# Optimization experiments

Measured on AMD Instinct MI355X. Metric: run time of the kernel, lower is better.

The kernel has to match this reference:

```python
import jax, jax.numpy as jnp
import numpy as np

MAX_SAMPLES = 400  # init max_samples
EPS = 1e-9


def setup_inputs() -> dict:
    key = jax.random.key(0)
    k1, k2, k3, k4 = jax.random.split(key, 4)
    E, N, K, L = 8192, 2048, 8, 16
    # per-edge probabilities (positive, as the loss takes log of ratios)
    probas = jax.random.uniform(k1, (E,), jnp.float32, minval=1e-3, maxval=1.0)
    # soft cluster assignments: row-normalized so Bhattacharyya coeff <= 1
    c = jax.random.uniform(k2, (N, K), jnp.float32)
    clusters = c / c.sum(axis=1, keepdims=True)
    edges_nn = jax.random.randint(k3, (E, 2), 0, N)
    label_keypoints = jax.random.randint(k4, (L,), 0, N)
    return {"probas": probas, "clusters": clusters,
            "edges_nn": edges_nn, "label_keypoints": label_keypoints}


def reference(probas, clusters, edges_nn, label_keypoints):
    E = edges_nn.shape[0]
    clst = jnp.argmax(clusters, axis=1)                      # [N] hard assignment
    c0 = clst[edges_nn[:, 0]]                                # [E]
    c1 = clst[edges_nn[:, 1]]                                # [E]
    assigned = clst[label_keypoints]                         # [L] clusters at keypoints
    # edge selected if either endpoint lies in a keypoint cluster (union over labels,
    # static-shape mask form of get_edges_on_location)
    sel = jnp.any((c0[None, :] == assigned[:, None]) |
                  (c1[None, :] == assigned[:, None]), axis=0)  # [E]
    sims = c0 == c1
    pos = sel & sims                                          # positive edges
    neg = sel & ~sims                                         # negative edges
    # Bhattacharyya coefficient per edge: sum_k sqrt(p_k * q_k)
    bc = jnp.sqrt(clusters[edges_nn[:, 0]] * clusters[edges_nn[:, 1]]).sum(axis=1)  # [E]
    # pos x neg cross product, restricted to pairs sharing the anchor node edges[.,0]
    same_anchor = edges_nn[:, 0][:, None] == edges_nn[None, :, 0]   # [E,E]
    valid = pos[:, None] & neg[None, :] & same_anchor               # [E,E]
    w = 1.0 - 0.5 * (bc[:, None] + bc[None, :])                     # [E,E] sampling prob
    logw = jnp.where(valid & (w > 0),
                     jnp.log(jnp.maximum(w, EPS)), -jnp.inf)
    # multinomial-without-replacement via Gumbel top-k (deterministic key)
    u = jax.random.uniform(jax.random.key(42), (E, E), jnp.float32)
    gumbel = -jnp.log(-jnp.log(u + EPS) + EPS)
    vals, flat_idx = jax.lax.top_k((logw + gumbel).reshape(-1), MAX_SAMPLES)
    i_ = flat_idx // E                                        # positive-edge rows
    j_ = flat_idx % E                                         # negative-edge rows
    p_pos = probas[i_]
    p_neg = probas[j_]
    term = jnp.log(p_pos / (p_pos + p_neg))                   # [max_samples]
    # guard against < max_samples valid pairs (torch would just sample fewer)
    ok = jnp.isfinite(vals)
    loss = -jnp.sum(jnp.where(ok, term, 0.0)) / jnp.maximum(jnp.sum(ok), 1)
    return loss
```

## Files before the change

kernel.cpp:

```cpp
#include <hip/hip_runtime.h>
#include <stdint.h>


#define E_CONST 8192
#define N_CONST 2048
#define K_CONST 8
#define L_CONST 16
#define MAXS 400
#define EPS_F 1e-9f
#define NTHR 1024
#define RCAP 4096
#define TCAP 6144

#define OFF_CLUA   0
#define OFF_CLUB   32768
#define OFF_PK     65536
#define OFF_Q      73728
#define OFF_CUR    81920
#define OFF_CSR    90112
#define OFF_BC     106496
#define OFF_CLST   139264
#define OFF_PA     141312
#define OFF_TMP    153600
#define OFF_HIST   153664
#define OFF_WSUM   154688
#define OFF_WCNT   154752
#define OFF_MISC   154816
#define LDS_BYTES  154848

struct Cand { float val; uint32_t pack; };

__device__ __forceinline__ uint2 threefry2x32_42(uint32_t x0, uint32_t x1) {
    const uint32_t ks0 = 0u, ks1 = 42u;
    const uint32_t ks2 = ks0 ^ ks1 ^ 0x1BD11BDAu;
    const uint32_t ks[3] = {ks0, ks1, ks2};
    const int R[2][4] = {{13, 15, 26, 6}, {17, 29, 16, 24}};
    x0 += ks0; x1 += ks1;
#pragma unroll
    for (int g = 0; g < 5; ++g) {
        const int* r = R[g & 1];
#pragma unroll
        for (int q = 0; q < 4; ++q) {
            x0 += x1;
            x1 = (x1 << r[q]) | (x1 >> (32 - r[q]));
            x1 ^= x0;
        }
        x0 += ks[(g + 1) % 3];
        x1 += ks[(g + 2) % 3] + (uint32_t)(g + 1);
    }
    return make_uint2(x0, x1);
}

__device__ __forceinline__ float gumbel_at(uint32_t idx) {
    uint2 o = threefry2x32_42(0u, idx);
    uint32_t bits = o.x ^ o.y;
    float u = __uint_as_float((bits >> 9) | 0x3F800000u) - 1.0f;
    return -__logf(-__logf(u + EPS_F) + EPS_F);
}

__device__ __forceinline__ uint32_t sortable_key(float f) {
    uint32_t b = __float_as_uint(f);
    return (b & 0x80000000u) ? ~b : (b | 0x80000000u);
}

__device__ __forceinline__ int argmax8(float4 a, float4 b) {
    float v[8] = {a.x, a.y, a.z, a.w, b.x, b.y, b.z, b.w};
    float best = v[0]; int bi = 0;
#pragma unroll
    for (int k = 1; k < 8; ++k)
        if (v[k] > best) { best = v[k]; bi = k; }
    return bi;
}

__device__ __forceinline__ void scan_inplace(int* arr, int* tmp, int* totalOut) {
    int tid = threadIdx.x;
    int lane = tid & 63, wid = tid >> 6;
    int i0 = 2 * tid, i1 = i0 + 1;
    int v0 = arr[i0], v1 = arr[i1];
    int s = v0 + v1;
    int inc = s;
#pragma unroll
    for (int off = 1; off < 64; off <<= 1) {
        int u = __shfl_up(inc, off);
        if (lane >= off) inc += u;
    }
    if (lane == 63) tmp[wid] = inc;
    __syncthreads();
    if (wid == 0) {
        int w = (lane < 16) ? tmp[lane] : 0;
        int incw = w;
#pragma unroll
        for (int off = 1; off < 16; off <<= 1) {
            int u = __shfl_up(incw, off);
            if (lane >= off) incw += u;
        }
        if (lane < 16) tmp[lane] = incw - w;
    }
    __syncthreads();
    int base = tmp[wid] + (inc - s);
    arr[i0] = base;
    arr[i1] = base + v0;
    if (tid == 1023) *totalOut = base + v0 + v1;
    __syncthreads();
}

__global__ __launch_bounds__(1024) void k_all(
    const float* __restrict__ probas, const float* __restrict__ clusters,
    const int* __restrict__ edges, const int* __restrict__ keypts,
    Cand* __restrict__ spill, int pmax, float* __restrict__ out) {

    extern __shared__ char smem[];
    float4*   s_cluA = (float4*)(smem + OFF_CLUA);
    float4*   s_cluB = (float4*)(smem + OFF_CLUB);
    int*      s_pk   = (int*)(smem + OFF_PK);
    int*      s_q    = (int*)(smem + OFF_Q);
    int*      s_cur  = (int*)(smem + OFF_CUR);
    uint16_t* s_csr  = (uint16_t*)(smem + OFF_CSR);
    float*    s_bc   = (float*)(smem + OFF_BC);
    uint8_t*  s_clst = (uint8_t*)(smem + OFF_CLST);
    uint16_t* s_pa   = (uint16_t*)(smem + OFF_PA);
    int*      s_tmp  = (int*)(smem + OFF_TMP);
    int*      s_hist = (int*)(smem + OFF_HIST);
    float*    s_wsum = (float*)(smem + OFF_WSUM);
    int*      s_wcnt = (int*)(smem + OFF_WCNT);
    int*      s_misc = (int*)(smem + OFF_MISC);

    int tid = threadIdx.x;

    const int2* ed2 = (const int2*)edges;
    int2 pre[8];
#pragma unroll
    for (int it = 0; it < 8; ++it) pre[it] = ed2[tid + it * NTHR];

    s_pk[tid] = 0; s_pk[tid + 1024] = 0;
    if (tid == 0) s_misc[0] = 0;

    const float4* c4 = (const float4*)clusters;
#pragma unroll
    for (int r = 0; r < 2; ++r) {
        int n = tid + r * 1024;
        float4 a = c4[2 * n], b = c4[2 * n + 1];
        s_cluA[n] = a; s_cluB[n] = b;
        s_clst[n] = (uint8_t)argmax8(a, b);
    }
    __syncthreads();
    if (tid < L_CONST)
        atomicOr((uint32_t*)&s_misc[0], 1u << s_clst[keypts[tid]]);
    __syncthreads();
    uint32_t m = (uint32_t)s_misc[0];

    uint32_t af[8];
#pragma unroll
    for (int it = 0; it < 8; ++it) {
        int e = tid + it * NTHR;
        int2 p = pre[it];
        int c0 = s_clst[p.x], c1 = s_clst[p.y];
        int f = 0;
        if ((((m >> c0) | (m >> c1)) & 1u)) f = (c0 == c1) ? 1 : 2;
        af[it] = ((uint32_t)p.x << 2) | (uint32_t)f;
        if (f == 1)      atomicAdd(&s_pk[p.x], 1);
        else if (f == 2) atomicAdd(&s_pk[p.x], 0x10000);
        float4 a0 = s_cluA[p.x], a1 = s_cluB[p.x];
        float4 b0 = s_cluA[p.y], b1 = s_cluB[p.y];
        float s = __builtin_amdgcn_sqrtf(a0.x * b0.x);
        s += __builtin_amdgcn_sqrtf(a0.y * b0.y);
        s += __builtin_amdgcn_sqrtf(a0.z * b0.z);
        s += __builtin_amdgcn_sqrtf(a0.w * b0.w);
        s += __builtin_amdgcn_sqrtf(a1.x * b1.x);
        s += __builtin_amdgcn_sqrtf(a1.y * b1.y);
        s += __builtin_amdgcn_sqrtf(a1.z * b1.z);
        s += __builtin_amdgcn_sqrtf(a1.w * b1.w);
        s_bc[e] = s;
    }
    __syncthreads();

    {
        int i0 = 2 * tid, i1 = i0 + 1;
        int p0 = s_pk[i0], p1 = s_pk[i1];
        s_q[i0] = (p0 & 0xFFFF) * (p0 >> 16);
        s_q[i1] = (p1 & 0xFFFF) * (p1 >> 16);
    }
    __syncthreads();
    scan_inplace(s_pk, s_tmp, &s_misc[1]);
    scan_inplace(s_q, s_tmp, &s_misc[2]);
    s_cur[2 * tid] = s_pk[2 * tid];
    s_cur[2 * tid + 1] = s_pk[2 * tid + 1];
    __syncthreads();
    int nPosTot = s_misc[1] & 0xFFFF;
    int nNegTot = s_misc[1] >> 16;
    int totQ = s_misc[2];
    int P = totQ; if (P > pmax) P = pmax;

#pragma unroll
    for (int it = 0; it < 8; ++it) {
        int f = (int)(af[it] & 3u);
        int a = (int)(af[it] >> 2);
        int e = tid + it * NTHR;
        if (f == 1) {
            int old = atomicAdd(&s_cur[a], 1);
            s_csr[old & 0xFFFF] = (uint16_t)e;
        } else if (f == 2) {
            int old = atomicAdd(&s_cur[a], 0x10000);
            s_csr[nPosTot + (old >> 16)] = (uint16_t)e;
        }
    }
    for (int a = tid; a < N_CONST; a += NTHR) {
        int q0 = s_q[a];
        int q1 = (a < N_CONST - 1) ? s_q[a + 1] : totQ;
        for (int t = q0; t < q1 && t < TCAP; ++t) s_pa[t] = (uint16_t)a;
    }
    __syncthreads();

    auto make_cand = [&](int t, float& val, uint32_t& pack) {
        int a;
        if (t < TCAP) a = (int)s_pa[t];
        else {
            int lo = 0, hi = N_CONST - 1;
#pragma unroll
            for (int itr = 0; itr < 11; ++itr) {
                int mid = (lo + hi + 1) >> 1;
                if (s_q[mid] <= t) lo = mid; else hi = mid - 1;
            }
            a = lo;
        }
        int loc = t - s_q[a];
        int pk = s_pk[a];
        int pb = pk & 0xFFFF, nb = pk >> 16;
        int nextN = (a < N_CONST - 1) ? (s_pk[a + 1] >> 16) : nNegTot;
        int nn = nextN - nb;
        int ip = loc / nn;
        int jn = loc - ip * nn;
        int i = s_csr[pb + ip];
        int j = s_csr[nPosTot + nb + jn];
        float w = 1.0f - 0.5f * (s_bc[i] + s_bc[j]);
        val = (w > 0.0f)
            ? __logf(fmaxf(w, EPS_F)) + gumbel_at((uint32_t)i * E_CONST + (uint32_t)j)
            : -INFINITY;
        pack = ((uint32_t)i << 16) | (uint32_t)j;
    };

    float vval0 = 0.f, vval1 = 0.f, vval2 = 0.f, vval3 = 0.f;
    uint32_t vpk0 = 0, vpk1 = 0, vpk2 = 0, vpk3 = 0;
    if (tid        < P) make_cand(tid,        vval0, vpk0);
    if (tid + 1024 < P) make_cand(tid + 1024, vval1, vpk1);
    if (tid + 2048 < P) make_cand(tid + 2048, vval2, vpk2);
    if (tid + 3072 < P) make_cand(tid + 3072, vval3, vpk3);
    for (int t = tid + RCAP; t < P; t += NTHR) {
        float v; uint32_t pk;
        make_cand(t, v, pk);
        spill[t - RCAP].val = v; spill[t - RCAP].pack = pk;
    }
    uint32_t vk0 = sortable_key(vval0), vk1 = sortable_key(vval1);
    uint32_t vk2 = sortable_key(vval2), vk3 = sortable_key(vval3);
    __syncthreads();

    uint32_t* s_prefix = (uint32_t*)&s_misc[3];
    int*      s_target = &s_misc[4];
    int M = P;
    uint32_t thr = 0;
    if (M > MAXS) {
        if (tid == 0) { *s_prefix = 0; *s_target = MAXS; }
        __syncthreads();
        for (int pass = 0; pass < 4; ++pass) {
            int shift = 24 - 8 * pass;
            if (tid < 256) s_hist[tid] = 0;
            __syncthreads();
            uint32_t pfx = *s_prefix;
            if (tid        < M && (pass == 0 || (vk0 >> (shift + 8)) == pfx)) atomicAdd(&s_hist[(vk0 >> shift) & 255], 1);
            if (tid + 1024 < M && (pass == 0 || (vk1 >> (shift + 8)) == pfx)) atomicAdd(&s_hist[(vk1 >> shift) & 255], 1);
            if (tid + 2048 < M && (pass == 0 || (vk2 >> (shift + 8)) == pfx)) atomicAdd(&s_hist[(vk2 >> shift) & 255], 1);
            if (tid + 3072 < M && (pass == 0 || (vk3 >> (shift + 8)) == pfx)) atomicAdd(&s_hist[(vk3 >> shift) & 255], 1);
            for (int t = tid + RCAP; t < M; t += NTHR) {
                uint32_t k = sortable_key(spill[t - RCAP].val);
                if (pass == 0 || (k >> (shift + 8)) == pfx)
                    atomicAdd(&s_hist[(k >> shift) & 255], 1);
            }
            __syncthreads();
            if (tid < 64) {
                int h0 = s_hist[4 * tid], h1 = s_hist[4 * tid + 1];
                int h2 = s_hist[4 * tid + 2], h3 = s_hist[4 * tid + 3];
                int sincl = h0 + h1 + h2 + h3;
#pragma unroll
                for (int off = 1; off < 64; off <<= 1) {
                    int v = __shfl_down(sincl, off);
                    if (tid + off < 64) sincl += v;
                }
                int excl = __shfl_down(sincl, 1);
                if (tid == 63) excl = 0;
                int suf3 = excl + h3;
                int suf2 = suf3 + h2;
                int suf1 = suf2 + h1;
                int suf0 = suf1 + h0;
                int tgt = *s_target;
                uint32_t pfxOld = *s_prefix;
                if      (suf0 >= tgt && suf1 < tgt) { *s_prefix = (pfxOld << 8) | (4u*tid+0); *s_target = tgt - suf1; }
                else if (suf1 >= tgt && suf2 < tgt) { *s_prefix = (pfxOld << 8) | (4u*tid+1); *s_target = tgt - suf2; }
                else if (suf2 >= tgt && suf3 < tgt) { *s_prefix = (pfxOld << 8) | (4u*tid+2); *s_target = tgt - suf3; }
                else if (suf3 >= tgt && excl < tgt) { *s_prefix = (pfxOld << 8) | (4u*tid+3); *s_target = tgt - excl; }
            }
            __syncthreads();
        }
        thr = *s_prefix;
    }

    float mysum = 0.f;
    int myc = 0;
    auto accum = [&](int t, float v, uint32_t k, uint32_t pk) {
        if (t < M && v != -INFINITY && k >= thr) {
            int i = (int)(pk >> 16), j = (int)(pk & 0xFFFFu);
            float pi = probas[i], pj = probas[j];
            mysum += __logf(pi / (pi + pj));
            myc++;
        }
    };
    accum(tid,        vval0, vk0, vpk0);
    accum(tid + 1024, vval1, vk1, vpk1);
    accum(tid + 2048, vval2, vk2, vpk2);
    accum(tid + 3072, vval3, vk3, vpk3);
    for (int t = tid + RCAP; t < M; t += NTHR) {
        Cand c = spill[t - RCAP];
        accum(t, c.val, sortable_key(c.val), c.pack);
    }
#pragma unroll
    for (int off = 32; off > 0; off >>= 1) {
        mysum += __shfl_down(mysum, off);
        myc   += __shfl_down(myc, off);
    }
    int wid = tid >> 6;
    if ((tid & 63) == 0) { s_wsum[wid] = mysum; s_wcnt[wid] = myc; }
    __syncthreads();
    if (tid == 0) {
        float s = 0.f; int c = 0;
        for (int w = 0; w < 16; ++w) { s += s_wsum[w]; c += s_wcnt[w]; }
        if (c < 1) c = 1;
        out[0] = -s / (float)c;
    }
}

extern "C" void kernel_launch(void* const* d_in, const int* in_sizes, int n_in,
                              void* d_out, int out_size, void* d_ws, size_t ws_size,
                              hipStream_t stream) {
    const float* probas   = (const float*)d_in[0];
    const float* clusters = (const float*)d_in[1];
    const int*   edges    = (const int*)d_in[2];
    const int*   keypts   = (const int*)d_in[3];
    float* out = (float*)d_out;

    Cand* spill = (Cand*)d_ws;
    int spill_cap = (int)(ws_size / sizeof(Cand));
    if (spill_cap > 61440) spill_cap = 61440;
    int pmax = RCAP + spill_cap;

    hipFuncSetAttribute((const void*)k_all,
                        hipFuncAttributeMaxDynamicSharedMemorySize, LDS_BYTES);

    k_all<<<1, NTHR, LDS_BYTES, stream>>>(probas, clusters, edges, keypts,
                                          spill, pmax, out);
}
```

Baseline: 26.22 us.

## Use 3-pass 11-bit radix select, stage probas in LDS, replace integer divide

The radix-select threshold search moves from four 8-bit passes to three passes of 11/11/10 bits. This cuts block-wide barriers and histogram rounds, but each pass now clears and scans a 2048-bin histogram, which reuses the s_cur region. The probas array is prefetched into registers early and written into the freed cluster LDS region, so the final accumulation reads LDS instead of doing random global loads. The per-candidate integer division is replaced by a float reciprocal estimate followed by correction loops.

Result: slower. 28.45 us (+8.5%).

```diff
diff --git a/kernel.cpp b/kernel.cpp
--- a/kernel.cpp
+++ b/kernel.cpp
@@ -22,11 +22,10 @@
 #define OFF_CLST   139264
 #define OFF_PA     141312
 #define OFF_TMP    153600
-#define OFF_HIST   153664
-#define OFF_WSUM   154688
-#define OFF_WCNT   154752
-#define OFF_MISC   154816
-#define LDS_BYTES  154848
+#define OFF_WSUM   153664
+#define OFF_WCNT   153728
+#define OFF_MISC   153792
+#define LDS_BYTES  153824
 
 struct Cand { float val; uint32_t pack; };
 
@@ -112,15 +111,16 @@
     extern __shared__ char smem[];
     float4*   s_cluA = (float4*)(smem + OFF_CLUA);
     float4*   s_cluB = (float4*)(smem + OFF_CLUB);
+    float*    s_prob = (float*)(smem + OFF_CLUA);
     int*      s_pk   = (int*)(smem + OFF_PK);
     int*      s_q    = (int*)(smem + OFF_Q);
     int*      s_cur  = (int*)(smem + OFF_CUR);
+    int*      s_hist = (int*)(smem + OFF_CUR);
     uint16_t* s_csr  = (uint16_t*)(smem + OFF_CSR);
     float*    s_bc   = (float*)(smem + OFF_BC);
     uint8_t*  s_clst = (uint8_t*)(smem + OFF_CLST);
     uint16_t* s_pa   = (uint16_t*)(smem + OFF_PA);
     int*      s_tmp  = (int*)(smem + OFF_TMP);
-    int*      s_hist = (int*)(smem + OFF_HIST);
     float*    s_wsum = (float*)(smem + OFF_WSUM);
     int*      s_wcnt = (int*)(smem + OFF_WCNT);
     int*      s_misc = (int*)(smem + OFF_MISC);
@@ -131,6 +131,8 @@
     int2 pre[8];
 #pragma unroll
     for (int it = 0; it < 8; ++it) pre[it] = ed2[tid + it * NTHR];
+    const float4* p4 = (const float4*)probas;
+    float4 pp0 = p4[tid], pp1 = p4[tid + 1024];
 
     s_pk[tid] = 0; s_pk[tid + 1024] = 0;
     if (tid == 0) s_misc[0] = 0;
@@ -209,6 +211,8 @@
         int q1 = (a < N_CONST - 1) ? s_q[a + 1] : totQ;
         for (int t = q0; t < q1 && t < TCAP; ++t) s_pa[t] = (uint16_t)a;
     }
+    ((float4*)s_prob)[tid] = pp0;
+    ((float4*)s_prob)[tid + 1024] = pp1;
     __syncthreads();
 
     auto make_cand = [&](int t, float& val, uint32_t& pack) {
@@ -228,7 +232,9 @@
         int pb = pk & 0xFFFF, nb = pk >> 16;
         int nextN = (a < N_CONST - 1) ? (s_pk[a + 1] >> 16) : nNegTot;
         int nn = nextN - nb;
-        int ip = loc / nn;
+        int ip = (int)((float)loc * __builtin_amdgcn_rcpf((float)nn));
+        while ((ip + 1) * nn <= loc) ++ip;
+        while (ip * nn > loc) --ip;
         int jn = loc - ip * nn;
         int i = s_csr[pb + ip];
         int j = s_csr[nPosTot + nb + jn];
@@ -260,26 +266,34 @@
     uint32_t thr = 0;
     if (M > MAXS) {
         if (tid == 0) { *s_prefix = 0; *s_target = MAXS; }
-        __syncthreads();
-        for (int pass = 0; pass < 4; ++pass) {
-            int shift = 24 - 8 * pass;
-            if (tid < 256) s_hist[tid] = 0;
+        for (int pass = 0; pass < 3; ++pass) {
+            const int shift = (pass == 0) ? 21 : (pass == 1) ? 10 : 0;
+            const uint32_t dmask = (pass == 2) ? 0x3FFu : 0x7FFu;
+            const int csh = (pass == 1) ? 21 : 10;
+            const int W = (pass == 2) ? 10 : 11;
+            s_hist[tid] = 0; s_hist[tid + 1024] = 0;
             __syncthreads();
             uint32_t pfx = *s_prefix;
-            if (tid        < M && (pass == 0 || (vk0 >> (shift + 8)) == pfx)) atomicAdd(&s_hist[(vk0 >> shift) & 255], 1);
-            if (tid + 1024 < M && (pass == 0 || (vk1 >> (shift + 8)) == pfx)) atomicAdd(&s_hist[(vk1 >> shift) & 255], 1);
-            if (tid + 2048 < M && (pass == 0 || (vk2 >> (shift + 8)) == pfx)) atomicAdd(&s_hist[(vk2 >> shift) & 255], 1);
-            if (tid + 3072 < M && (pass == 0 || (vk3 >> (shift + 8)) == pfx)) atomicAdd(&s_hist[(vk3 >> shift) & 255], 1);
+            auto hist_add = [&](bool inr, uint32_t k) {
+                if (!inr) return;
+                if (pass != 0 && (k >> csh) != pfx) return;
+                atomicAdd(&s_hist[(k >> shift) & dmask], 1);
+            };
+            hist_add(tid        < M, vk0);
+            hist_add(tid + 1024 < M, vk1);
+            hist_add(tid + 2048 < M, vk2);
+            hist_add(tid + 3072 < M, vk3);
             for (int t = tid + RCAP; t < M; t += NTHR) {
                 uint32_t k = sortable_key(spill[t - RCAP].val);
-                if (pass == 0 || (k >> (shift + 8)) == pfx)
-                    atomicAdd(&s_hist[(k >> shift) & 255], 1);
+                if (pass == 0 || (k >> csh) == pfx)
+                    atomicAdd(&s_hist[(k >> shift) & dmask], 1);
             }
             __syncthreads();
             if (tid < 64) {
-                int h0 = s_hist[4 * tid], h1 = s_hist[4 * tid + 1];
-                int h2 = s_hist[4 * tid + 2], h3 = s_hist[4 * tid + 3];
-                int sincl = h0 + h1 + h2 + h3;
+                int h[32]; int lsum = 0;
+#pragma unroll
+                for (int b = 0; b < 32; ++b) { h[b] = s_hist[32 * tid + b]; lsum += h[b]; }
+                int sincl = lsum;
 #pragma unroll
                 for (int off = 1; off < 64; off <<= 1) {
                     int v = __shfl_down(sincl, off);
@@ -287,16 +301,20 @@
                 }
                 int excl = __shfl_down(sincl, 1);
                 if (tid == 63) excl = 0;
-                int suf3 = excl + h3;
-                int suf2 = suf3 + h2;
-                int suf1 = suf2 + h1;
-                int suf0 = suf1 + h0;
                 int tgt = *s_target;
                 uint32_t pfxOld = *s_prefix;
-                if      (suf0 >= tgt && suf1 < tgt) { *s_prefix = (pfxOld << 8) | (4u*tid+0); *s_target = tgt - suf1; }
-                else if (suf1 >= tgt && suf2 < tgt) { *s_prefix = (pfxOld << 8) | (4u*tid+1); *s_target = tgt - suf2; }
-                else if (suf2 >= tgt && suf3 < tgt) { *s_prefix = (pfxOld << 8) | (4u*tid+2); *s_target = tgt - suf3; }
-                else if (suf3 >= tgt && excl < tgt) { *s_prefix = (pfxOld << 8) | (4u*tid+3); *s_target = tgt - excl; }
+                if (sincl >= tgt && excl < tgt) {
+                    int acc = excl;
+#pragma unroll
+                    for (int b = 31; b >= 0; --b) {
+                        acc += h[b];
+                        if (acc >= tgt) {
+                            *s_prefix = (pfxOld << W) | (uint32_t)(32 * tid + b);
+                            *s_target = tgt - (acc - h[b]);
+                            break;
+                        }
+                    }
+                }
             }
             __syncthreads();
         }
@@ -308,7 +326,7 @@
     auto accum = [&](int t, float v, uint32_t k, uint32_t pk) {
         if (t < M && v != -INFINITY && k >= thr) {
             int i = (int)(pk >> 16), j = (int)(pk & 0xFFFFu);
-            float pi = probas[i], pj = probas[j];
+            float pi = s_prob[i], pj = s_prob[j];
             mysum += __logf(pi / (pi + pj));
             myc++;
         }
```
